# Performance work log

Measured on AMD Instinct MI355X. Metric: run time of the kernel, lower is better.

## Reference

```python
import jax, jax.numpy as jnp
import numpy as np

B, S, DIM = 2, 2048, 2048
NH, NKV = 16, 8
HD = DIM // NH  # 128
ROPE_THETA = 10000.0


def setup_inputs() -> dict:
    key = jax.random.key(0)
    ks = jax.random.split(key, 7)
    std = DIM ** -0.5
    x = jax.random.normal(ks[0], (B, S, DIM), jnp.float32)
    wq = jax.random.normal(ks[1], (NH * HD, DIM), jnp.float32) * std
    wk = jax.random.normal(ks[2], (NKV * HD, DIM), jnp.float32) * std
    wv = jax.random.normal(ks[3], (NKV * HD, DIM), jnp.float32) * std
    wo = jax.random.normal(ks[4], (DIM, NH * HD), jnp.float32) * std
    inv_freq = 1.0 / (ROPE_THETA ** (jnp.arange(0, HD, 2, dtype=jnp.float32) / HD))
    ang = jnp.arange(S, dtype=jnp.float32)[:, None] * inv_freq[None, :]  # [S, HD//2]
    freqs_cos = jnp.cos(ang)
    freqs_sin = jnp.sin(ang)
    # diffusion-style random per-batch token mask: t ~ U[0,1) per batch row
    t = jax.random.uniform(ks[5], (B, 1))
    mask = jax.random.uniform(ks[6], (B, S)) < t  # True = masked key
    mask = mask.at[:, 0].set(False)  # first token never masked
    return dict(x=x, wq=wq, wk=wk, wv=wv, wo=wo,
                freqs_cos=freqs_cos, freqs_sin=freqs_sin, mask=mask)


def _rope(x, cos, sin):
    # x: [b, s, h, d]; pairs (x[2i], x[2i+1]) rotated by angle[s, i]
    xr, xi = x[..., 0::2], x[..., 1::2]
    c = cos[None, :, None, :]
    s = sin[None, :, None, :]
    out = jnp.stack([xr * c - xi * s, xr * s + xi * c], axis=-1)
    return out.reshape(x.shape)


def reference(x, wq, wk, wv, wo, freqs_cos, freqs_sin, mask):
    b, s, _ = x.shape
    xq = jnp.einsum('bsd,ed->bse', x, wq).reshape(b, s, NH, HD)
    xk = jnp.einsum('bsd,ed->bse', x, wk).reshape(b, s, NKV, HD)
    xv = jnp.einsum('bsd,ed->bse', x, wv).reshape(b, s, NKV, HD)
    xq = _rope(xq, freqs_cos, freqs_sin)
    xk = _rope(xk, freqs_cos, freqs_sin)
    n_rep = NH // NKV
    xk = jnp.repeat(xk, n_rep, axis=2)  # repeat_kv (GQA)
    xv = jnp.repeat(xv, n_rep, axis=2)
    q = xq.transpose(0, 2, 1, 3)  # [b, h, s, d]
    k = xk.transpose(0, 2, 1, 3)
    v = xv.transpose(0, 2, 1, 3)
    scale = 1.0 / np.sqrt(HD).astype(np.float32)
    scores = jnp.einsum('bhqd,bhkd->bhqk', q, k) * scale  # [b, h, s, s]
    scores = jnp.where(mask[:, None, None, :], -jnp.inf, scores)
    probs = jax.nn.softmax(scores, axis=-1)
    out = jnp.einsum('bhqk,bhkd->bhqd', probs, v)
    out = out.transpose(0, 2, 1, 3).reshape(b, s, NH * HD)
    return jnp.einsum('bse,de->bsd', out, wo)
```

## Files before the change

### kernel.cpp

```cpp
#include <hip/hip_runtime.h>
#include <hip/hip_bf16.h>
#include <cstdint>
#include <cstddef>

#define S_LEN   2048
#define NHQ     16
#define NKV_H   8
#define HD_DIM  128
#define DMODEL  2048
#define BATCH   2
#define KVD     (NKV_H * HD_DIM)
#define QKV_LD  4096

typedef float f32x4  __attribute__((ext_vector_type(4)));
typedef __bf16 bf16x8 __attribute__((ext_vector_type(8)));
typedef __bf16 bf16x4 __attribute__((ext_vector_type(4)));

__device__ __forceinline__ void gload_lds16(const __bf16* g, __bf16* l) {
    __builtin_amdgcn_global_load_lds(
        (const __attribute__((address_space(1))) void*)g,
        (__attribute__((address_space(3))) void*)l, 16, 0, 0);
}

__global__ void sniff_x_kernel(const unsigned* __restrict__ x,
                               int* __restrict__ flag) {
    __shared__ int cnt;
    if (threadIdx.x == 0) cnt = 0;
    __syncthreads();
    int c = 0;
    for (int j = threadIdx.x; j < 1024; j += 256) {
        unsigned hw = x[j] & 0xFFFFu;
        unsigned e  = (hw >> 7) & 0xFF;
        if (hw == 0u || (e >= 118 && e <= 132)) c++;
    }
    atomicAdd(&cnt, c);
    __syncthreads();
    if (threadIdx.x == 0) *flag = (cnt > 512) ? 1 : 0;
}

__global__ void sniff_fc_kernel(const unsigned* __restrict__ fc,
                                int* __restrict__ flag) {
    if (threadIdx.x == 0) *flag = (fc[0] == 0x3F803F80u) ? 1 : 0;
}

__global__ void mask_norm_kernel(const unsigned char* __restrict__ mraw,
                                 unsigned char* __restrict__ mout, int n) {
    __shared__ int f_bf16, f_f32, f_u8;
    if (threadIdx.x == 0) { f_bf16 = 0; f_f32 = 0; f_u8 = 0; }
    __syncthreads();
    const unsigned* dw = (const unsigned*)mraw;
    int ndw = n / 4;
    for (int j = threadIdx.x; j < ndw; j += blockDim.x) {
        unsigned v = dw[j];
        if (v == 0x00003F80u || v == 0x3F803F80u) f_bf16 = 1;
        else if (v == 0x3F800000u) f_f32 = 1;
        else if (v & 0xFFFFFFFEu) f_u8 = 1;
    }
    __syncthreads();
    int layout;
    if (f_bf16) layout = 3;
    else if (f_f32) layout = 2;
    else if (f_u8) layout = 0;
    else layout = 1;
    for (int i = threadIdx.x; i < n; i += blockDim.x) {
        unsigned v;
        if (layout == 0)      v = mraw[i];
        else if (layout == 3) v = ((const unsigned short*)mraw)[i];
        else                  v = ((const unsigned*)mraw)[i];
        mout[i] = v ? 1u : 0u;
    }
}

__global__ __launch_bounds__(256)
void conv_bf16_kernel(const void* __restrict__ src, __bf16* __restrict__ dst,
                      int n8, const int* __restrict__ dflag) {
    int i = blockIdx.x * blockDim.x + threadIdx.x;
    if (i >= n8) return;
    size_t off = (size_t)i * 8;
    if (*dflag) {
        *reinterpret_cast<uint4*>(dst + off) =
            *reinterpret_cast<const uint4*>((const __bf16*)src + off);
    } else {
        const float* f = (const float*)src + off;
        float4 a = *reinterpret_cast<const float4*>(f);
        float4 b = *reinterpret_cast<const float4*>(f + 4);
        bf16x8 v;
        v[0] = (__bf16)a.x; v[1] = (__bf16)a.y; v[2] = (__bf16)a.z; v[3] = (__bf16)a.w;
        v[4] = (__bf16)b.x; v[5] = (__bf16)b.y; v[6] = (__bf16)b.z; v[7] = (__bf16)b.w;
        *reinterpret_cast<bf16x8*>(dst + off) = v;
    }
}

__global__ __launch_bounds__(256)
void conv_bf16_strided_kernel(const void* __restrict__ src,
                              __bf16* __restrict__ dstbase,
                              int n8, const int* __restrict__ dflag) {
    int i = blockIdx.x * blockDim.x + threadIdx.x;
    if (i >= n8) return;
    size_t off = (size_t)i * 8;
    size_t row = off >> 11;
    size_t col = off & 2047;
    __bf16* dst = dstbase + row * QKV_LD + col;
    if (*dflag) {
        *reinterpret_cast<uint4*>(dst) =
            *reinterpret_cast<const uint4*>((const __bf16*)src + off);
    } else {
        const float* f = (const float*)src + off;
        float4 a = *reinterpret_cast<const float4*>(f);
        float4 b = *reinterpret_cast<const float4*>(f + 4);
        bf16x8 v;
        v[0] = (__bf16)a.x; v[1] = (__bf16)a.y; v[2] = (__bf16)a.z; v[3] = (__bf16)a.w;
        v[4] = (__bf16)b.x; v[5] = (__bf16)b.y; v[6] = (__bf16)b.z; v[7] = (__bf16)b.w;
        *reinterpret_cast<bf16x8*>(dst) = v;
    }
}

template <bool OUT_BF16>
__global__ __launch_bounds__(256)
void gemm_bt_async(const __bf16* __restrict__ A, const __bf16* __restrict__ Bw,
                   void* __restrict__ Cv, int K, int lda, int ldb, int ldc) {
    __shared__ __align__(16) __bf16 As[128 * 64];
    __shared__ __align__(16) __bf16 Bs[128 * 64];

    const int t    = threadIdx.x;
    const int w    = t >> 6;
    const int lane = t & 63;
    const int quad = lane >> 4;
    const int l16  = lane & 15;
    const int wm   = (w >> 1) * 64;
    const int wn   = (w & 1) * 64;

    const int nwg  = gridDim.x * gridDim.y;
    const int lin  = blockIdx.y * gridDim.x + blockIdx.x;
    const int swz  = (lin & 7) * (nwg >> 3) + (lin >> 3);
    const int m0   = (swz % gridDim.x) * 128;
    const int n0   = (swz / gridDim.x) * 128;

    const int rl   = lane >> 3;
    const int gl   = lane & 7;

    f32x4 acc[4][4];
#pragma unroll
    for (int i = 0; i < 4; ++i)
#pragma unroll
        for (int j = 0; j < 4; ++j) acc[i][j] = (f32x4){0.f, 0.f, 0.f, 0.f};

    for (int k0 = 0; k0 < K; k0 += 64) {
        __syncthreads();
#pragma unroll
        for (int p = 0; p < 4; ++p) {
            const int rowb = w * 32 + p * 8;
            const int r    = rowb + rl;
            const int gA   = gl ^ rl;
            gload_lds16(A  + (size_t)(m0 + r) * lda + k0 + gA * 8, &As[rowb * 64]);
            gload_lds16(Bw + (size_t)(n0 + r) * ldb + k0 + gA * 8, &Bs[rowb * 64]);
        }
        __syncthreads();
#pragma unroll
        for (int ks = 0; ks < 2; ++ks) {
            const int G = ks * 4 + quad;
            const int gsw = (G ^ (l16 & 7)) * 8;
            bf16x8 af[4], bf[4];
#pragma unroll
            for (int i = 0; i < 4; ++i)
                af[i] = *reinterpret_cast<const bf16x8*>(
                    &As[(wm + i * 16 + l16) * 64 + gsw]);
#pragma unroll
            for (int j = 0; j < 4; ++j)
                bf[j] = *reinterpret_cast<const bf16x8*>(
                    &Bs[(wn + j * 16 + l16) * 64 + gsw]);
#pragma unroll
            for (int i = 0; i < 4; ++i)
#pragma unroll
                for (int j = 0; j < 4; ++j)
                    acc[i][j] = __builtin_amdgcn_mfma_f32_16x16x32_bf16(
                        af[i], bf[j], acc[i][j], 0, 0, 0);
        }
    }
#pragma unroll
    for (int i = 0; i < 4; ++i)
#pragma unroll
        for (int r = 0; r < 4; ++r) {
            size_t m = (size_t)(m0 + wm + i * 16 + quad * 4 + r);
#pragma unroll
            for (int j = 0; j < 4; ++j) {
                int n = n0 + wn + j * 16 + l16;
                if constexpr (OUT_BF16)
                    ((__hip_bfloat16*)Cv)[m * ldc + n] = __float2bfloat16(acc[i][j][r]);
                else
                    ((float*)Cv)[m * ldc + n] = acc[i][j][r];
            }
        }
}

__global__ void rope_kernel(__hip_bfloat16* __restrict__ xqk,
                            const void* __restrict__ cosv,
                            const void* __restrict__ sinv,
                            const int* __restrict__ dflag_fc,
                            int npairs) {
    int idx = blockIdx.x * blockDim.x + threadIdx.x;
    if (idx >= npairs) return;
    int i  = idx & 63;
    int h  = (idx >> 6) % 24;
    int bs = idx / (64 * 24);
    int s  = bs & (S_LEN - 1);
    float c, sn;
    if (*dflag_fc) {
        c  = __bfloat162float(((const __hip_bfloat16*)cosv)[s * 64 + i]);
        sn = __bfloat162float(((const __hip_bfloat16*)sinv)[s * 64 + i]);
    } else {
        c  = ((const float*)cosv)[s * 64 + i];
        sn = ((const float*)sinv)[s * 64 + i];
    }
    unsigned* p = (unsigned*)(xqk + (size_t)bs * QKV_LD + h * HD_DIM) + i;
    unsigned u = *p;
    float xr = __uint_as_float(u << 16);
    float xi = __uint_as_float(u & 0xFFFF0000u);
    float o0 = xr * c - xi * sn;
    float o1 = xr * sn + xi * c;
    union { __hip_bfloat16 h2[2]; unsigned u32; } out;
    out.h2[0] = __float2bfloat16(o0);
    out.h2[1] = __float2bfloat16(o1);
    *p = out.u32;
}

__global__ __launch_bounds__(256)
void transpose_v_kernel(const __hip_bfloat16* __restrict__ xv,
                        __hip_bfloat16* __restrict__ vt) {
    __shared__ unsigned short T[32][36];
    const int t  = threadIdx.x;
    const int s0 = blockIdx.x * 32;
    const int d0 = blockIdx.y * 32;
    const int z  = blockIdx.z;
    const int b  = z >> 3;
    const int kv = z & 7;
    {
        int sr = t >> 3, dc = (t & 7) * 4;
        const unsigned short* p = (const unsigned short*)xv
            + (size_t)(b * S_LEN + s0 + sr) * QKV_LD + kv * 128 + d0 + dc;
        uint2 v = *reinterpret_cast<const uint2*>(p);
        T[sr][dc + 0] = (unsigned short)(v.x & 0xFFFFu);
        T[sr][dc + 1] = (unsigned short)(v.x >> 16);
        T[sr][dc + 2] = (unsigned short)(v.y & 0xFFFFu);
        T[sr][dc + 3] = (unsigned short)(v.y >> 16);
    }
    __syncthreads();
    {
        int dr = t >> 3, sc = (t & 7) * 4;
        unsigned w0 = (unsigned)T[sc + 0][dr] | ((unsigned)T[sc + 1][dr] << 16);
        unsigned w1 = (unsigned)T[sc + 2][dr] | ((unsigned)T[sc + 3][dr] << 16);
        unsigned short* q = (unsigned short*)vt
            + ((size_t)z * 128 + d0 + dr) * S_LEN + s0 + sc;
        uint2 v; v.x = w0; v.y = w1;
        *reinterpret_cast<uint2*>(q) = v;
    }
}

__global__ __launch_bounds__(256)
void attn_mfma2_kernel(__hip_bfloat16* qkv,
                       const __hip_bfloat16* __restrict__ vt_g,
                       const unsigned char* __restrict__ msk) {
    __shared__ __align__(16) __bf16 Ks[64 * 128];
    __shared__ __align__(16) __bf16 Vt[128 * 64];
    __shared__ __align__(16) __bf16 Ps[4][32][64];

    const int t    = threadIdx.x;
    const int w    = t >> 6;
    const int lane = t & 63;
    const int quad = lane >> 4;
    const int l16  = lane & 15;

    const int bid = ((blockIdx.x & 7) << 6) | (blockIdx.x >> 3);
    const int qt  = bid & 15;
    const int h   = (bid >> 4) & (NHQ - 1);
    const int b   = bid >> 8;
    const int kvh = h >> 1;
    const int q0  = qt * 128;

    bf16x8 qf[2][4];
    {
        const __bf16* qrow = (const __bf16*)qkv
            + (size_t)(b * S_LEN + q0 + w * 32 + l16) * QKV_LD + h * 128 + quad * 8;
#pragma unroll
        for (int g = 0; g < 2; ++g)
#pragma unroll
            for (int ks = 0; ks < 4; ++ks)
                qf[g][ks] = *reinterpret_cast<const bf16x8*>(
                    qrow + (size_t)g * 16 * QKV_LD + ks * 32);
    }

    float m_r[2], l_r[2];
    f32x4 o[2][8];
#pragma unroll
    for (int g = 0; g < 2; ++g) {
        m_r[g] = -INFINITY; l_r[g] = 0.f;
#pragma unroll
        for (int d0 = 0; d0 < 8; ++d0) o[g][d0] = (f32x4){0.f, 0.f, 0.f, 0.f};
    }

    const float scale2 = 0.08838834764831845f * 1.4426950408889634f;
    const int gbase = lane & 48;

    const __bf16* kp[4];
    const __bf16* vp[4];
    {
        const __bf16* xk = (const __bf16*)qkv + 2048;
        const int krl = lane >> 4, kgl = lane & 15;
        const int vrl = lane >> 3, vgl = lane & 7;
#pragma unroll
        for (int p = 0; p < 4; ++p) {
            const int row = w * 16 + p * 4 + krl;
            kp[p] = xk + (size_t)(b * S_LEN + row) * QKV_LD
                       + kvh * 128 + (kgl ^ (row & 7)) * 8;
        }
#pragma unroll
        for (int p = 0; p < 4; ++p) {
            const int row = w * 32 + p * 8 + vrl;
            vp[p] = (const __bf16*)vt_g
                  + ((size_t)(b * NKV_H + kvh) * 128 + row) * S_LEN
                  + (vgl ^ (row & 7)) * 8;
        }
    }
    const unsigned char* mbase = msk + b * S_LEN;

    for (int k0 = 0; k0 < S_LEN; k0 += 64) {
        __syncthreads();
#pragma unroll
        for (int p = 0; p < 4; ++p)
            gload_lds16(kp[p], &Ks[(w * 16 + p * 4) * 128]);
#pragma unroll
        for (int p = 0; p < 4; ++p)
            gload_lds16(vp[p], &Vt[(w * 32 + p * 8) * 64]);
#pragma unroll
        for (int p = 0; p < 4; ++p) { kp[p] += 64 * QKV_LD; vp[p] += 64; }

        unsigned mk4[4];
        {
            const unsigned* mp = (const unsigned*)(mbase + k0);
#pragma unroll
            for (int n0 = 0; n0 < 4; ++n0) mk4[n0] = mp[n0 * 4 + quad];
        }
        __syncthreads();

        f32x4 sc[2][4];
#pragma unroll
        for (int g = 0; g < 2; ++g)
#pragma unroll
            for (int n0 = 0; n0 < 4; ++n0) sc[g][n0] = (f32x4){0.f, 0.f, 0.f, 0.f};
        __builtin_amdgcn_s_setprio(1);
#pragma unroll
        for (int ks = 0; ks < 4; ++ks) {
            const int G = ks * 4 + quad;
#pragma unroll
            for (int n0 = 0; n0 < 4; ++n0) {
                const int row  = n0 * 16 + l16;
                const int slot = G ^ (row & 7);
                bf16x8 kf = *reinterpret_cast<const bf16x8*>(&Ks[row * 128 + slot * 8]);
                sc[0][n0] = __builtin_amdgcn_mfma_f32_16x16x32_bf16(kf, qf[0][ks], sc[0][n0], 0, 0, 0);
                sc[1][n0] = __builtin_amdgcn_mfma_f32_16x16x32_bf16(kf, qf[1][ks], sc[1][n0], 0, 0, 0);
            }
        }
        __builtin_amdgcn_s_setprio(0);

        float rm[2];
#pragma unroll
        for (int g = 0; g < 2; ++g) {
#pragma unroll
            for (int n0 = 0; n0 < 4; ++n0)
#pragma unroll
                for (int r = 0; r < 4; ++r)
                    sc[g][n0][r] = ((mk4[n0] >> (r * 8)) & 0xFF) ? -INFINITY : sc[g][n0][r];
            float tq0 = fmaxf(fmaxf(sc[g][0][0], sc[g][0][1]), fmaxf(sc[g][0][2], sc[g][0][3]));
            float tq1 = fmaxf(fmaxf(sc[g][1][0], sc[g][1][1]), fmaxf(sc[g][1][2], sc[g][1][3]));
            float tq2 = fmaxf(fmaxf(sc[g][2][0], sc[g][2][1]), fmaxf(sc[g][2][2], sc[g][2][3]));
            float tq3 = fmaxf(fmaxf(sc[g][3][0], sc[g][3][1]), fmaxf(sc[g][3][2], sc[g][3][3]));
            float m4 = fmaxf(fmaxf(tq0, tq1), fmaxf(tq2, tq3));
            m4 = fmaxf(m4, __shfl_xor(m4, 16, 64));
            m4 = fmaxf(m4, __shfl_xor(m4, 32, 64));
            rm[g] = m4;
        }

        bool need = ((rm[0] - m_r[0]) * scale2 > 8.0f) ||
                    ((rm[1] - m_r[1]) * scale2 > 8.0f);
        if (__any((int)need)) {
#pragma unroll
            for (int g = 0; g < 2; ++g) {
                float mn = fmaxf(m_r[g], rm[g]);
                float al = exp2f((m_r[g] - mn) * scale2);
                m_r[g] = mn;
                l_r[g] *= al;
                float alq[4];
#pragma unroll
                for (int r = 0; r < 4; ++r)
                    alq[r] = __shfl(al, gbase | (quad * 4 + r), 64);
#pragma unroll
                for (int d0 = 0; d0 < 8; ++d0)
#pragma unroll
                    for (int r = 0; r < 4; ++r) o[g][d0][r] *= alq[r];
            }
        }

#pragma unroll
        for (int g = 0; g < 2; ++g) {
            float negm = -m_r[g] * scale2;
#pragma unroll
            for (int n0 = 0; n0 < 4; ++n0) {
#pragma unroll
                for (int r = 0; r < 4; ++r) {
                    float p = exp2f(fmaf(sc[g][n0][r], scale2, negm));
                    sc[g][n0][r] = p;
                    l_r[g] += p;
                }
                const int kb    = n0 * 16 + quad * 4;
                const int gran  = kb >> 3;
                const int half4 = kb & 4;
                const int slot  = gran ^ (l16 & 7);
                bf16x4 pk;
                pk[0] = (__bf16)sc[g][n0][0];
                pk[1] = (__bf16)sc[g][n0][1];
                pk[2] = (__bf16)sc[g][n0][2];
                pk[3] = (__bf16)sc[g][n0][3];
                *reinterpret_cast<bf16x4*>(&Ps[w][g * 16 + l16][slot * 8 + half4]) = pk;
            }
        }

        __builtin_amdgcn_s_setprio(1);
#pragma unroll
        for (int kk = 0; kk < 64; kk += 32) {
            const int Gp    = (kk >> 3) + quad;
            const int slotp = Gp ^ (l16 & 7);
            bf16x8 af0 = *reinterpret_cast<const bf16x8*>(&Ps[w][l16][slotp * 8]);
            bf16x8 af1 = *reinterpret_cast<const bf16x8*>(&Ps[w][16 + l16][slotp * 8]);
#pragma unroll
            for (int d0 = 0; d0 < 8; ++d0) {
                const int row  = d0 * 16 + l16;
                const int slot = Gp ^ (row & 7);
                bf16x8 bf = *reinterpret_cast<const bf16x8*>(&Vt[row * 64 + slot * 8]);
                o[0][d0] = __builtin_amdgcn_mfma_f32_16x16x32_bf16(af0, bf, o[0][d0], 0, 0, 0);
                o[1][d0] = __builtin_amdgcn_mfma_f32_16x16x32_bf16(af1, bf, o[1][d0], 0, 0, 0);
            }
        }
        __builtin_amdgcn_s_setprio(0);
    }

    __hip_bfloat16* att = qkv;
#pragma unroll
    for (int g = 0; g < 2; ++g) {
        float ls = l_r[g];
        ls += __shfl_xor(ls, 16, 64);
        ls += __shfl_xor(ls, 32, 64);
        float invl = 1.f / ls;
        float invq[4];
#pragma unroll
        for (int r = 0; r < 4; ++r)
            invq[r] = __shfl(invl, gbase | (quad * 4 + r), 64);
#pragma unroll
        for (int d0 = 0; d0 < 8; ++d0)
#pragma unroll
            for (int r = 0; r < 4; ++r) {
                size_t row = (size_t)(b * S_LEN + q0 + w * 32 + g * 16 + quad * 4 + r);
                att[row * QKV_LD + h * 128 + d0 * 16 + l16] =
                    __float2bfloat16(o[g][d0][r] * invq[r]);
            }
    }
}

extern "C" void kernel_launch(void* const* d_in, const int* in_sizes, int n_in,
                              void* d_out, int out_size, void* d_ws, size_t ws_size,
                              hipStream_t stream) {
    const void* x  = d_in[0];
    const void* wq = d_in[1];
    const void* wk = d_in[2];
    const void* wv = d_in[3];
    const void* wo = d_in[4];
    const void* fc = d_in[5];
    const void* fs = d_in[6];
    const unsigned char* mraw = (const unsigned char*)d_in[7];

    const int M = BATCH * S_LEN;
    char* wsb = (char*)d_ws;
    int* dflag_x  = (int*)wsb;
    int* dflag_fc = (int*)(wsb + 64);
    unsigned char* mnorm = (unsigned char*)(wsb + 128);
    __hip_bfloat16* qkv = (__hip_bfloat16*)(wsb + 8192);

    char* dob = (char*)d_out;
    __bf16* xb    = (__bf16*)dob;
    __bf16* wcomb = (__bf16*)(dob + (16u << 20));
    __bf16* wqb = wcomb;
    __bf16* wkb = wcomb + (size_t)2048 * 2048;
    __bf16* wvb = wcomb + (size_t)3072 * 2048;
    __hip_bfloat16* vt = (__hip_bfloat16*)d_out;

    hipLaunchKernelGGL(sniff_x_kernel, dim3(1), dim3(256), 0, stream,
                       (const unsigned*)x, dflag_x);
    hipLaunchKernelGGL(sniff_fc_kernel, dim3(1), dim3(64), 0, stream,
                       (const unsigned*)fc, dflag_fc);
    hipLaunchKernelGGL(mask_norm_kernel, dim3(1), dim3(256), 0, stream,
                       mraw, mnorm, BATCH * S_LEN);

    hipLaunchKernelGGL(conv_bf16_kernel, dim3((M * DMODEL / 8) / 256), dim3(256), 0, stream,
                       x, xb, M * DMODEL / 8, dflag_x);
    hipLaunchKernelGGL(conv_bf16_kernel, dim3((DMODEL * DMODEL / 8) / 256), dim3(256), 0, stream,
                       wq, wqb, DMODEL * DMODEL / 8, dflag_x);
    hipLaunchKernelGGL(conv_bf16_kernel, dim3((KVD * DMODEL / 8) / 256), dim3(256), 0, stream,
                       wk, wkb, KVD * DMODEL / 8, dflag_x);
    hipLaunchKernelGGL(conv_bf16_kernel, dim3((KVD * DMODEL / 8) / 256), dim3(256), 0, stream,
                       wv, wvb, KVD * DMODEL / 8, dflag_x);

    hipLaunchKernelGGL((gemm_bt_async<true>), dim3(M / 128, QKV_LD / 128), dim3(256), 0, stream,
                       xb, wcomb, (void*)qkv, DMODEL, DMODEL, DMODEL, QKV_LD);

    int npairs = M * 24 * (HD_DIM / 2);
    hipLaunchKernelGGL(rope_kernel, dim3(npairs / 256), dim3(256), 0, stream,
                       qkv, fc, fs, dflag_fc, npairs);

    hipLaunchKernelGGL(transpose_v_kernel, dim3(S_LEN / 32, HD_DIM / 32, BATCH * NKV_H),
                       dim3(256), 0, stream, qkv + 3072, vt);

    hipLaunchKernelGGL(attn_mfma2_kernel, dim3(BATCH * NHQ * (S_LEN / 128)), dim3(256), 0, stream,
                       qkv, vt, mnorm);

    hipLaunchKernelGGL(conv_bf16_strided_kernel, dim3((DMODEL * DMODEL / 8) / 256), dim3(256), 0, stream,
                       wo, (__bf16*)qkv + 2048, DMODEL * DMODEL / 8, dflag_x);

    hipLaunchKernelGGL((gemm_bt_async<false>), dim3(M / 128, DMODEL / 128), dim3(256), 0, stream,
                       (const __bf16*)qkv, (const __bf16*)qkv + 2048, d_out,
                       DMODEL, QKV_LD, QKV_LD, DMODEL);
}
```

Measured before the change: 468.5 us.

## Merge prep and conversion kernels, overlap K/V tile loads in attention

```diff
diff --git a/kernel.cpp b/kernel.cpp
--- a/kernel.cpp
+++ b/kernel.cpp
@@ -22,62 +22,57 @@
         (__attribute__((address_space(3))) void*)l, 16, 0, 0);
 }
 
-__global__ void sniff_x_kernel(const unsigned* __restrict__ x,
-                               int* __restrict__ flag) {
-    __shared__ int cnt;
-    if (threadIdx.x == 0) cnt = 0;
-    __syncthreads();
-    int c = 0;
-    for (int j = threadIdx.x; j < 1024; j += 256) {
-        unsigned hw = x[j] & 0xFFFFu;
-        unsigned e  = (hw >> 7) & 0xFF;
-        if (hw == 0u || (e >= 118 && e <= 132)) c++;
-    }
-    atomicAdd(&cnt, c);
-    __syncthreads();
-    if (threadIdx.x == 0) *flag = (cnt > 512) ? 1 : 0;
-}
-
-__global__ void sniff_fc_kernel(const unsigned* __restrict__ fc,
-                                int* __restrict__ flag) {
-    if (threadIdx.x == 0) *flag = (fc[0] == 0x3F803F80u) ? 1 : 0;
-}
-
-__global__ void mask_norm_kernel(const unsigned char* __restrict__ mraw,
-                                 unsigned char* __restrict__ mout, int n) {
-    __shared__ int f_bf16, f_f32, f_u8;
-    if (threadIdx.x == 0) { f_bf16 = 0; f_f32 = 0; f_u8 = 0; }
-    __syncthreads();
-    const unsigned* dw = (const unsigned*)mraw;
-    int ndw = n / 4;
-    for (int j = threadIdx.x; j < ndw; j += blockDim.x) {
-        unsigned v = dw[j];
-        if (v == 0x00003F80u || v == 0x3F803F80u) f_bf16 = 1;
-        else if (v == 0x3F800000u) f_f32 = 1;
-        else if (v & 0xFFFFFFFEu) f_u8 = 1;
-    }
-    __syncthreads();
-    int layout;
-    if (f_bf16) layout = 3;
-    else if (f_f32) layout = 2;
-    else if (f_u8) layout = 0;
-    else layout = 1;
-    for (int i = threadIdx.x; i < n; i += blockDim.x) {
-        unsigned v;
-        if (layout == 0)      v = mraw[i];
-        else if (layout == 3) v = ((const unsigned short*)mraw)[i];
-        else                  v = ((const unsigned*)mraw)[i];
-        mout[i] = v ? 1u : 0u;
-    }
-}
-
 __global__ __launch_bounds__(256)
-void conv_bf16_kernel(const void* __restrict__ src, __bf16* __restrict__ dst,
-                      int n8, const int* __restrict__ dflag) {
-    int i = blockIdx.x * blockDim.x + threadIdx.x;
-    if (i >= n8) return;
-    size_t off = (size_t)i * 8;
-    if (*dflag) {
+void prep_kernel(const unsigned* __restrict__ x, int* __restrict__ flag_x,
+                 const unsigned* __restrict__ fc, int* __restrict__ flag_fc,
+                 const unsigned char* __restrict__ mraw,
+                 unsigned char* __restrict__ mout, int n) {
+    if (blockIdx.x == 0) {
+        __shared__ int cnt;
+        if (threadIdx.x == 0) cnt = 0;
+        __syncthreads();
+        int c = 0;
+        for (int j = threadIdx.x; j < 1024; j += 256) {
+            unsigned hw = x[j] & 0xFFFFu;
+            unsigned e  = (hw >> 7) & 0xFF;
+            if (hw == 0u || (e >= 118 && e <= 132)) c++;
+        }
+        atomicAdd(&cnt, c);
+        __syncthreads();
+        if (threadIdx.x == 0) *flag_x = (cnt > 512) ? 1 : 0;
+    } else if (blockIdx.x == 1) {
+        if (threadIdx.x == 0) *flag_fc = (fc[0] == 0x3F803F80u) ? 1 : 0;
+    } else {
+        __shared__ int f_bf16, f_f32, f_u8;
+        if (threadIdx.x == 0) { f_bf16 = 0; f_f32 = 0; f_u8 = 0; }
+        __syncthreads();
+        const unsigned* dw = (const unsigned*)mraw;
+        int ndw = n / 4;
+        for (int j = threadIdx.x; j < ndw; j += blockDim.x) {
+            unsigned v = dw[j];
+            if (v == 0x00003F80u || v == 0x3F803F80u) f_bf16 = 1;
+            else if (v == 0x3F800000u) f_f32 = 1;
+            else if (v & 0xFFFFFFFEu) f_u8 = 1;
+        }
+        __syncthreads();
+        int layout;
+        if (f_bf16) layout = 3;
+        else if (f_f32) layout = 2;
+        else if (f_u8) layout = 0;
+        else layout = 1;
+        for (int i = threadIdx.x; i < n; i += blockDim.x) {
+            unsigned v;
+            if (layout == 0)      v = mraw[i];
+            else if (layout == 3) v = ((const unsigned short*)mraw)[i];
+            else                  v = ((const unsigned*)mraw)[i];
+            mout[i] = v ? 1u : 0u;
+        }
+    }
+}
+
+__device__ __forceinline__ void conv8(const void* src, __bf16* dst,
+                                      size_t off, int isbf16) {
+    if (isbf16) {
         *reinterpret_cast<uint4*>(dst + off) =
             *reinterpret_cast<const uint4*>((const __bf16*)src + off);
     } else {
@@ -88,6 +83,24 @@
         v[0] = (__bf16)a.x; v[1] = (__bf16)a.y; v[2] = (__bf16)a.z; v[3] = (__bf16)a.w;
         v[4] = (__bf16)b.x; v[5] = (__bf16)b.y; v[6] = (__bf16)b.z; v[7] = (__bf16)b.w;
         *reinterpret_cast<bf16x8*>(dst + off) = v;
+    }
+}
+
+__global__ __launch_bounds__(256)
+void conv_all_kernel(const void* __restrict__ x,  const void* __restrict__ wq,
+                     const void* __restrict__ wk, const void* __restrict__ wv,
+                     __bf16* __restrict__ xb, __bf16* __restrict__ wcomb,
+                     const int* __restrict__ dflag) {
+    int i = blockIdx.x * 256 + threadIdx.x;
+    int isb = *dflag;
+    if (i < 1048576) {
+        conv8(x, xb, (size_t)i * 8, isb);
+    } else if (i < 1572864) {
+        conv8(wq, wcomb, (size_t)(i - 1048576) * 8, isb);
+    } else if (i < 1835008) {
+        conv8(wk, wcomb + (size_t)2048 * 2048, (size_t)(i - 1572864) * 8, isb);
+    } else {
+        conv8(wv, wcomb + (size_t)3072 * 2048, (size_t)(i - 1835008) * 8, isb);
     }
 }
 
@@ -323,16 +336,26 @@
     }
     const unsigned char* mbase = msk + b * S_LEN;
 
+    auto stage_K = [&]() {
+#pragma unroll
+        for (int p = 0; p < 4; ++p) {
+            gload_lds16(kp[p], &Ks[(w * 16 + p * 4) * 128]);
+            kp[p] += 64 * QKV_LD;
+        }
+    };
+    auto stage_V = [&]() {
+#pragma unroll
+        for (int p = 0; p < 4; ++p) {
+            gload_lds16(vp[p], &Vt[(w * 32 + p * 8) * 64]);
+            vp[p] += 64;
+        }
+    };
+
+    stage_K();
+    __syncthreads();
+
     for (int k0 = 0; k0 < S_LEN; k0 += 64) {
-        __syncthreads();
-#pragma unroll
-        for (int p = 0; p < 4; ++p)
-            gload_lds16(kp[p], &Ks[(w * 16 + p * 4) * 128]);
-#pragma unroll
-        for (int p = 0; p < 4; ++p)
-            gload_lds16(vp[p], &Vt[(w * 32 + p * 8) * 64]);
-#pragma unroll
-        for (int p = 0; p < 4; ++p) { kp[p] += 64 * QKV_LD; vp[p] += 64; }
+        stage_V();
 
         unsigned mk4[4];
         {
@@ -340,7 +363,6 @@
 #pragma unroll
             for (int n0 = 0; n0 < 4; ++n0) mk4[n0] = mp[n0 * 4 + quad];
         }
-        __syncthreads();
 
         f32x4 sc[2][4];
 #pragma unroll
@@ -361,6 +383,10 @@
             }
         }
         __builtin_amdgcn_s_setprio(0);
+
+        __syncthreads();
+
+        if (k0 + 64 < S_LEN) stage_K();
 
         float rm[2];
 #pragma unroll
@@ -441,6 +467,8 @@
             }
         }
         __builtin_amdgcn_s_setprio(0);
+
+        __syncthreads();
     }
 
     __hip_bfloat16* att = qkv;
@@ -487,26 +515,14 @@
     char* dob = (char*)d_out;
     __bf16* xb    = (__bf16*)dob;
     __bf16* wcomb = (__bf16*)(dob + (16u << 20));
-    __bf16* wqb = wcomb;
-    __bf16* wkb = wcomb + (size_t)2048 * 2048;
-    __bf16* wvb = wcomb + (size_t)3072 * 2048;
     __hip_bfloat16* vt = (__hip_bfloat16*)d_out;
 
-    hipLaunchKernelGGL(sniff_x_kernel, dim3(1), dim3(256), 0, stream,
-                       (const unsigned*)x, dflag_x);
-    hipLaunchKernelGGL(sniff_fc_kernel, dim3(1), dim3(64), 0, stream,
-                       (const unsigned*)fc, dflag_fc);
-    hipLaunchKernelGGL(mask_norm_kernel, dim3(1), dim3(256), 0, stream,
+    hipLaunchKernelGGL(prep_kernel, dim3(3), dim3(256), 0, stream,
+                       (const unsigned*)x, dflag_x, (const unsigned*)fc, dflag_fc,
                        mraw, mnorm, BATCH * S_LEN);
 
-    hipLaunchKernelGGL(conv_bf16_kernel, dim3((M * DMODEL / 8) / 256), dim3(256), 0, stream,
-                       x, xb, M * DMODEL / 8, dflag_x);
-    hipLaunchKernelGGL(conv_bf16_kernel, dim3((DMODEL * DMODEL / 8) / 256), dim3(256), 0, stream,
-                       wq, wqb, DMODEL * DMODEL / 8, dflag_x);
-    hipLaunchKernelGGL(conv_bf16_kernel, dim3((KVD * DMODEL / 8) / 256), dim3(256), 0, stream,
-                       wk, wkb, KVD * DMODEL / 8, dflag_x);
-    hipLaunchKernelGGL(conv_bf16_kernel, dim3((KVD * DMODEL / 8) / 256), dim3(256), 0, stream,
-                       wv, wvb, KVD * DMODEL / 8, dflag_x);
+    hipLaunchKernelGGL(conv_all_kernel, dim3(8192), dim3(256), 0, stream,
+                       x, wq, wk, wv, xb, wcomb, dflag_x);
 
     hipLaunchKernelGGL((gemm_bt_async<true>), dim3(M / 128, QKV_LD / 128), dim3(256), 0, stream,
                        xb, wcomb, (void*)qkv, DMODEL, DMODEL, DMODEL, QKV_LD);
```

After: 455.3 us. 1.03x faster.
